# Performance work log

Hardware: AMD Instinct MI355X
Metric: run time of the kernel (lower is better)

The kernel has to match this reference:

```python
import jax, jax.numpy as jnp
import numpy as np

B, S, HID = 1, 2048, 2048
NH, NKV, D = 32, 8, 64
GROUPS = NH // NKV
THETA = 10000.0


def _rope_tables(seq_len, dim):
    inv_freq = 1.0 / (THETA ** (jnp.arange(0, dim, 2, dtype=jnp.float32) / dim))
    t = jnp.arange(seq_len, dtype=jnp.float32)
    freqs = jnp.outer(t, inv_freq)            # [S, D/2]
    emb = jnp.concatenate([freqs, freqs], axis=-1)  # [S, D]
    return jnp.cos(emb), jnp.sin(emb)


def _rotate_half(x):
    x1, x2 = jnp.split(x, 2, axis=-1)
    return jnp.concatenate([-x2, x1], axis=-1)


def setup_inputs() -> dict:
    key = jax.random.key(0)
    ks = jax.random.split(key, 8)
    hidden_states = jax.random.normal(ks[0], (B, S, HID), dtype=jnp.float32)
    # additive causal mask, 0 on/below diagonal, -1e9 above
    causal = jnp.tril(jnp.ones((S, S), dtype=bool))
    attention_mask = jnp.where(causal, 0.0, -1e9).astype(jnp.float32)[None, None]
    sc = 0.02
    Wq = sc * jax.random.normal(ks[1], (NH * D, HID), dtype=jnp.float32)
    bq = jnp.zeros((NH * D,), dtype=jnp.float32)
    Wk = sc * jax.random.normal(ks[2], (NKV * D, HID), dtype=jnp.float32)
    bk = jnp.zeros((NKV * D,), dtype=jnp.float32)
    Wv = sc * jax.random.normal(ks[3], (NKV * D, HID), dtype=jnp.float32)
    bv = jnp.zeros((NKV * D,), dtype=jnp.float32)
    Wo = sc * jax.random.normal(ks[4], (HID, NH * D), dtype=jnp.float32)
    return {"hidden_states": hidden_states, "attention_mask": attention_mask,
            "Wq": Wq, "bq": bq, "Wk": Wk, "bk": bk, "Wv": Wv, "bv": bv, "Wo": Wo}


def reference(hidden_states, attention_mask, Wq, bq, Wk, bk, Wv, bv, Wo):
    b, s, _ = hidden_states.shape
    q = (hidden_states @ Wq.T + bq).reshape(b, s, NH, D).transpose(0, 2, 1, 3)   # [B,NH,S,D]
    k = (hidden_states @ Wk.T + bk).reshape(b, s, NKV, D).transpose(0, 2, 1, 3)  # [B,NKV,S,D]
    v = (hidden_states @ Wv.T + bv).reshape(b, s, NKV, D).transpose(0, 2, 1, 3)
    cos, sin = _rope_tables(s, D)
    cos = cos[None, None]; sin = sin[None, None]
    q = q * cos + _rotate_half(q) * sin
    k = k * cos + _rotate_half(k) * sin
    # GQA: repeat KV heads to match query heads
    k = jnp.repeat(k, GROUPS, axis=1)  # [B,NH,S,D]
    v = jnp.repeat(v, GROUPS, axis=1)
    scores = jnp.einsum('bhqd,bhkd->bhqk', q, k) / jnp.sqrt(jnp.float32(D))
    scores = jnp.clip(scores, -50.0, 50.0)
    scores = scores + attention_mask
    probs = jax.nn.softmax(scores.astype(jnp.float32), axis=-1).astype(q.dtype)
    attn = jnp.einsum('bhqk,bhkd->bhqd', probs, v)
    attn = attn.transpose(0, 2, 1, 3).reshape(b, s, NH * D)
    return attn @ Wo.T
```

## Files before the change

### kernel.cpp

```cpp
#include <hip/hip_runtime.h>
#include <hip/hip_bf16.h>
#include <stdint.h>

typedef unsigned short u16;
typedef unsigned int u32;

#define S_LEN 2048
#define HID 2048
#define NH 32
#define NKV 8
#define HD 64
#define PIT 2080

using f32x4 = __attribute__((ext_vector_type(4))) float;
using bfrag = __attribute__((ext_vector_type(8))) short;

__device__ __forceinline__ float b2f(u16 u) {
  union { u32 i; float f; } c; c.i = ((u32)u) << 16; return c.f;
}
__device__ __forceinline__ u16 f2b(float f) {
  union { float f; u32 i; } c; c.f = f;
  u32 r = c.i + 0x7fffu + ((c.i >> 16) & 1u);
  return (u16)(r >> 16);
}
__device__ __forceinline__ uint4 cvt8(const float* __restrict__ p) {
  float4 a = *(const float4*)p;
  float4 b = *(const float4*)(p + 4);
  uint4 r;
  r.x = (u32)f2b(a.x) | ((u32)f2b(a.y) << 16);
  r.y = (u32)f2b(a.z) | ((u32)f2b(a.w) << 16);
  r.z = (u32)f2b(b.x) | ((u32)f2b(b.y) << 16);
  r.w = (u32)f2b(b.z) | ((u32)f2b(b.w) << 16);
  return r;
}

__device__ __forceinline__ void gl2lds16(const u16* g, u16* l) {
  __builtin_amdgcn_global_load_lds(
      (const __attribute__((address_space(1))) void*)g,
      (__attribute__((address_space(3))) void*)l,
      16, 0, 0);
}

__global__ void conv_all(const float* __restrict__ hid, const float* __restrict__ Wq,
                         const float* __restrict__ Wk, const float* __restrict__ Wv,
                         u16* __restrict__ hidb, u16* __restrict__ Wqkvb) {
  int row = blockIdx.x;
  int col = threadIdx.x * 8;
  const float* src; u16* dst;
  if (row < 2048)      { src = hid + (size_t)row * 2048;          dst = hidb  + (size_t)row * PIT; }
  else if (row < 4096) { src = Wq + (size_t)(row - 2048) * 2048;  dst = Wqkvb + (size_t)(row - 2048) * PIT; }
  else if (row < 4608) { src = Wk + (size_t)(row - 4096) * 2048;  dst = Wqkvb + (size_t)(row - 4096 + 2048) * PIT; }
  else                 { src = Wv + (size_t)(row - 4608) * 2048;  dst = Wqkvb + (size_t)(row - 4608 + 2560) * PIT; }
  *(uint4*)(dst + col) = cvt8(src + col);
}

__global__ void conv_f2b_p(const float* __restrict__ in, u16* __restrict__ out, int n8) {
  int i = blockIdx.x * 256 + threadIdx.x;
  if (i >= n8) return;
  int row = i >> 8;
  int col = (i & 255) * 8;
  *(uint4*)(out + (size_t)row * PIT + col) = cvt8(in + (size_t)row * 2048 + col);
}

__global__ __launch_bounds__(256, 3) void gemm_qkv(
    const u16* __restrict__ A, const u16* __restrict__ B,
    const float* __restrict__ bq, const float* __restrict__ bk, const float* __restrict__ bv,
    u16* __restrict__ Qb, u16* __restrict__ Kb, u16* __restrict__ Vt)
{
  __shared__ __align__(16) u16 As[64 * 32];
  __shared__ __align__(16) u16 Bs[128 * 32];
  __shared__ u16 strip_s[4][16 * 72];

  const int tid  = threadIdx.x;
  const int m0   = blockIdx.y * 64;
  const int n0   = blockIdx.x * 128;
  const int lane = tid & 63;
  const int w    = tid >> 6;
  const int wm   = w >> 1, wn = w & 1;
  const int quad = lane >> 4, l16 = lane & 15;

  const int srow = tid >> 2;
  const int scol = (tid & 3) * 8;
  const u16* ga = A + (size_t)(m0 + srow) * PIT + scol;
  const u16* gb = B + (size_t)(n0 + srow) * PIT + scol;
  u16* la = As + tid * 8;
  u16* lb = Bs + tid * 8;

  f32x4 zero = {0.f, 0.f, 0.f, 0.f};
  f32x4 acc[2][4];
#pragma unroll
  for (int mi = 0; mi < 2; ++mi)
#pragma unroll
    for (int ni = 0; ni < 4; ++ni) acc[mi][ni] = zero;

  for (int k0 = 0; k0 < HID; k0 += 32) {
    __syncthreads();
    gl2lds16(ga + k0, la);
    gl2lds16(gb + k0, lb);
    gl2lds16(gb + (size_t)64 * PIT + k0, lb + 2048);
    __syncthreads();

    bfrag af[2], bf[4];
#pragma unroll
    for (int i = 0; i < 2; ++i)
      af[i] = *(const bfrag*)&As[(wm * 32 + i * 16 + l16) * 32 + quad * 8];
#pragma unroll
    for (int i = 0; i < 4; ++i)
      bf[i] = *(const bfrag*)&Bs[(wn * 64 + i * 16 + l16) * 32 + quad * 8];
#pragma unroll
    for (int mi = 0; mi < 2; ++mi)
#pragma unroll
      for (int ni = 0; ni < 4; ++ni)
        acc[mi][ni] = __builtin_amdgcn_mfma_f32_16x16x32_bf16(af[mi], bf[ni], acc[mi][ni], 0, 0, 0);
  }

  u16* strip = strip_s[w];
  const int rr = lane >> 2;
  const int co = (lane & 3) * 8;

  if (n0 < 2048) {
#pragma unroll
    for (int mi = 0; mi < 2; ++mi) {
#pragma unroll
      for (int n01 = 0; n01 < 2; ++n01)
#pragma unroll
        for (int i = 0; i < 4; ++i) {
          int d  = n01 * 16 + l16;
          int c1 = n0 + wn * 64 + d;
          float x1 = acc[mi][n01][i]     + bq[c1];
          float x2 = acc[mi][n01 + 2][i] + bq[c1 + 32];
          float inv = exp2f(-(float)d * 0.41524101186092034f);
          float ang = (float)(m0 + wm * 32 + mi * 16 + quad * 4 + i) * inv;
          float cs = cosf(ang), sn = sinf(ang);
          strip[(quad * 4 + i) * 72 + d]      = f2b(x1 * cs - x2 * sn);
          strip[(quad * 4 + i) * 72 + d + 32] = f2b(x2 * cs + x1 * sn);
        }
      uint4 v0 = *(const uint4*)&strip[rr * 72 + co];
      uint4 v1 = *(const uint4*)&strip[rr * 72 + 32 + co];
      size_t gb2 = (size_t)(m0 + wm * 32 + mi * 16 + rr) * 2048 + n0 + wn * 64;
      *(uint4*)(Qb + gb2 + co)      = v0;
      *(uint4*)(Qb + gb2 + 32 + co) = v1;
    }
  } else if (n0 < 2560) {
    int cb = (n0 - 2048) + wn * 64;
#pragma unroll
    for (int mi = 0; mi < 2; ++mi) {
#pragma unroll
      for (int n01 = 0; n01 < 2; ++n01)
#pragma unroll
        for (int i = 0; i < 4; ++i) {
          int d  = n01 * 16 + l16;
          int cg = cb + d;
          float x1 = acc[mi][n01][i]     + bk[cg];
          float x2 = acc[mi][n01 + 2][i] + bk[cg + 32];
          float inv = exp2f(-(float)d * 0.41524101186092034f);
          float ang = (float)(m0 + wm * 32 + mi * 16 + quad * 4 + i) * inv;
          float cs = cosf(ang), sn = sinf(ang);
          strip[(quad * 4 + i) * 72 + d]      = f2b(x1 * cs - x2 * sn);
          strip[(quad * 4 + i) * 72 + d + 32] = f2b(x2 * cs + x1 * sn);
        }
      uint4 v0 = *(const uint4*)&strip[rr * 72 + co];
      uint4 v1 = *(const uint4*)&strip[rr * 72 + 32 + co];
      size_t gb2 = (size_t)(m0 + wm * 32 + mi * 16 + rr) * 512 + cb;
      *(uint4*)(Kb + gb2 + co)      = v0;
      *(uint4*)(Kb + gb2 + 32 + co) = v1;
    }
  } else {
    int cgb = (n0 - 2560) + wn * 64;
#pragma unroll
    for (int ni = 0; ni < 4; ++ni) {
      float bvv = bv[cgb + ni * 16 + l16];
#pragma unroll
      for (int mi = 0; mi < 2; ++mi)
#pragma unroll
        for (int i = 0; i < 4; ++i)
          strip[l16 * 72 + mi * 16 + quad * 4 + i] = f2b(acc[mi][ni][i] + bvv);
      uint4 v0 = *(const uint4*)&strip[rr * 72 + co];
      size_t gb2 = (size_t)(cgb + ni * 16 + rr) * PIT + m0 + wm * 32;
      *(uint4*)(Vt + gb2 + co) = v0;
    }
  }
}

__global__ __launch_bounds__(256, 3) void gemm_o(
    const u16* __restrict__ A, const u16* __restrict__ B, float* __restrict__ C)
{
  __shared__ __align__(16) u16 As[64 * 32];
  __shared__ __align__(16) u16 Bs[128 * 32];

  const int tid  = threadIdx.x;
  const int m0   = blockIdx.y * 64;
  const int n0   = blockIdx.x * 128;
  const int lane = tid & 63;
  const int w    = tid >> 6;
  const int wm   = w >> 1, wn = w & 1;
  const int quad = lane >> 4, l16 = lane & 15;

  const int srow = tid >> 2;
  const int scol = (tid & 3) * 8;
  const u16* ga = A + (size_t)(m0 + srow) * PIT + scol;
  const u16* gb = B + (size_t)(n0 + srow) * PIT + scol;
  u16* la = As + tid * 8;
  u16* lb = Bs + tid * 8;

  f32x4 zero = {0.f, 0.f, 0.f, 0.f};
  f32x4 acc[2][4];
#pragma unroll
  for (int mi = 0; mi < 2; ++mi)
#pragma unroll
    for (int ni = 0; ni < 4; ++ni) acc[mi][ni] = zero;

  for (int k0 = 0; k0 < HID; k0 += 32) {
    __syncthreads();
    gl2lds16(ga + k0, la);
    gl2lds16(gb + k0, lb);
    gl2lds16(gb + (size_t)64 * PIT + k0, lb + 2048);
    __syncthreads();

    bfrag af[2], bf[4];
#pragma unroll
    for (int i = 0; i < 2; ++i)
      af[i] = *(const bfrag*)&As[(wm * 32 + i * 16 + l16) * 32 + quad * 8];
#pragma unroll
    for (int i = 0; i < 4; ++i)
      bf[i] = *(const bfrag*)&Bs[(wn * 64 + i * 16 + l16) * 32 + quad * 8];
#pragma unroll
    for (int mi = 0; mi < 2; ++mi)
#pragma unroll
      for (int ni = 0; ni < 4; ++ni)
        acc[mi][ni] = __builtin_amdgcn_mfma_f32_16x16x32_bf16(af[mi], bf[ni], acc[mi][ni], 0, 0, 0);
  }

#pragma unroll
  for (int ni = 0; ni < 4; ++ni) {
    int col = n0 + wn * 64 + ni * 16 + l16;
#pragma unroll
    for (int mi = 0; mi < 2; ++mi)
#pragma unroll
      for (int i = 0; i < 4; ++i) {
        int row = m0 + wm * 32 + mi * 16 + quad * 4 + i;
        C[(size_t)row * 2048 + col] = acc[mi][ni][i];
      }
  }
}

#define SM_SC 0.18033688011112042f
#define SM_UB 72.134752044448169f

__global__ __launch_bounds__(256, 2) void attn_flash3(
    const u16* __restrict__ Qb, const u16* __restrict__ Kb,
    const u16* __restrict__ Vt, u16* __restrict__ Ab)
{
  __shared__ u16 Ps[4][2][16][72];

  const int h    = blockIdx.x;
  const int qbb  = 15 - (int)blockIdx.y;
  const int kvh  = h >> 2;
  const int tid  = threadIdx.x;
  const int lane = tid & 63;
  const int w    = tid >> 6;
  const int quad = lane >> 4, l16 = lane & 15;

  bfrag qf[2][2];
#pragma unroll
  for (int g = 0; g < 2; ++g) {
    const u16* qp = Qb + (size_t)(qbb * 128 + g * 64 + w * 16 + l16) * 2048 + h * 64 + quad * 8;
    qf[g][0] = *(const bfrag*)qp;
    qf[g][1] = *(const bfrag*)(qp + 32);
  }

  const u16* Kbase = Kb + (size_t)l16 * 512 + kvh * 64 + quad * 8;
  const u16* Vbase = Vt + (size_t)(kvh * 64 + l16) * PIT + quad * 8;

  f32x4 zero = {0.f, 0.f, 0.f, 0.f};
  f32x4 o_acc[2][4];
  float lpart[2][4];
#pragma unroll
  for (int g = 0; g < 2; ++g)
#pragma unroll
    for (int nb = 0; nb < 4; ++nb) { o_acc[g][nb] = zero; lpart[g][nb] = 0.f; }

#define LOADKV(kb, k0, k1, v0, v1)                                              \
  do {                                                                          \
    _Pragma("unroll")                                                           \
    for (int nb = 0; nb < 4; ++nb) {                                            \
      const u16* kp = Kbase + (size_t)((kb) * 64 + nb * 16) * 512;              \
      k0[nb] = *(const bfrag*)kp;                                               \
      k1[nb] = *(const bfrag*)(kp + 32);                                        \
      const u16* vp = Vbase + (size_t)(nb * 16) * PIT + (kb) * 64;              \
      v0[nb] = *(const bfrag*)vp;                                               \
      v1[nb] = *(const bfrag*)(vp + 32);                                        \
    }                                                                           \
  } while (0)

#define QKT_SM_FULL(k0, k1, g)                                                  \
  do {                                                                          \
    f32x4 s_acc[4];                                                             \
    _Pragma("unroll")                                                           \
    for (int nb = 0; nb < 4; ++nb) {                                            \
      s_acc[nb] = __builtin_amdgcn_mfma_f32_16x16x32_bf16(qf[g][0], k0[nb], zero, 0, 0, 0); \
      s_acc[nb] = __builtin_amdgcn_mfma_f32_16x16x32_bf16(qf[g][1], k1[nb], s_acc[nb], 0, 0, 0); \
    }                                                                           \
    _Pragma("unroll")                                                           \
    for (int nb = 0; nb < 4; ++nb)                                              \
      _Pragma("unroll")                                                         \
      for (int i = 0; i < 4; ++i) {                                             \
        float u = s_acc[nb][i] * SM_SC;                                         \
        u = fminf(SM_UB, fmaxf(-SM_UB, u));                                     \
        float p = __builtin_amdgcn_exp2f(u);                                    \
        lpart[g][i] += p;                                                       \
        Ps[w][g][quad * 4 + i][nb * 16 + l16] = f2b(p);                         \
      }                                                                         \
  } while (0)

#define QKT_SM_DIAG(k0, k1, g)                                                  \
  do {                                                                          \
    f32x4 s_acc[4];                                                             \
    _Pragma("unroll")                                                           \
    for (int nb = 0; nb < 4; ++nb) {                                            \
      s_acc[nb] = __builtin_amdgcn_mfma_f32_16x16x32_bf16(qf[g][0], k0[nb], zero, 0, 0, 0); \
      s_acc[nb] = __builtin_amdgcn_mfma_f32_16x16x32_bf16(qf[g][1], k1[nb], s_acc[nb], 0, 0, 0); \
    }                                                                           \
    _Pragma("unroll")                                                           \
    for (int nb = 0; nb < 4; ++nb)                                              \
      _Pragma("unroll")                                                         \
      for (int i = 0; i < 4; ++i) {                                             \
        float u = s_acc[nb][i] * SM_SC;                                         \
        u = fminf(SM_UB, fmaxf(-SM_UB, u));                                     \
        bool msk = (nb * 16 + l16 > w * 16 + quad * 4 + i);                     \
        float p = msk ? 0.0f : __builtin_amdgcn_exp2f(u);                       \
        lpart[g][i] += p;                                                       \
        Ps[w][g][quad * 4 + i][nb * 16 + l16] = f2b(p);                         \
      }                                                                         \
  } while (0)

#define PVACC(v0, v1, g)                                                        \
  do {                                                                          \
    bfrag pf0 = *(const bfrag*)&Ps[w][g][l16][quad * 8];                        \
    bfrag pf1 = *(const bfrag*)&Ps[w][g][l16][32 + quad * 8];                   \
    _Pragma("unroll")                                                           \
    for (int nb = 0; nb < 4; ++nb) {                                            \
      o_acc[g][nb] = __builtin_amdgcn_mfma_f32_16x16x32_bf16(pf0, v0[nb], o_acc[g][nb], 0, 0, 0); \
      o_acc[g][nb] = __builtin_amdgcn_mfma_f32_16x16x32_bf16(pf1, v1[nb], o_acc[g][nb], 0, 0, 0); \
    }                                                                           \
  } while (0)

  bfrag kX0[4], kX1[4], vX0[4], vX1[4];
  bfrag kY0[4], kY1[4], vY0[4], vY1[4];

  const int bulk  = 2 * qbb;
  const int kbmax = bulk + 1;

  LOADKV(0, kX0, kX1, vX0, vX1);

  int kb = 0;
  while (kb + 2 <= bulk) {
    LOADKV(kb + 1, kY0, kY1, vY0, vY1);
    QKT_SM_FULL(kX0, kX1, 0);
    QKT_SM_FULL(kX0, kX1, 1);
    PVACC(vX0, vX1, 0);
    PVACC(vX0, vX1, 1);
    LOADKV(kb + 2, kX0, kX1, vX0, vX1);
    QKT_SM_FULL(kY0, kY1, 0);
    QKT_SM_FULL(kY0, kY1, 1);
    PVACC(vY0, vY1, 0);
    PVACC(vY0, vY1, 1);
    kb += 2;
  }
  LOADKV(kbmax, kY0, kY1, vY0, vY1);
  QKT_SM_DIAG(kX0, kX1, 0);
  QKT_SM_FULL(kX0, kX1, 1);
  PVACC(vX0, vX1, 0);
  PVACC(vX0, vX1, 1);
  QKT_SM_DIAG(kY0, kY1, 1);
  PVACC(vY0, vY1, 1);

#pragma unroll
  for (int off = 1; off < 16; off <<= 1)
#pragma unroll
    for (int g = 0; g < 2; ++g)
#pragma unroll
      for (int i = 0; i < 4; ++i)
        lpart[g][i] += __shfl_xor(lpart[g][i], off, 64);

#pragma unroll
  for (int g = 0; g < 2; ++g)
#pragma unroll
    for (int i = 0; i < 4; ++i) {
      float inv = 1.0f / lpart[g][i];
      size_t rbase = (size_t)(qbb * 128 + g * 64 + w * 16 + quad * 4 + i) * PIT + h * 64;
#pragma unroll
      for (int nb = 0; nb < 4; ++nb)
        Ab[rbase + nb * 16 + l16] = f2b(o_acc[g][nb][i] * inv);
    }
}

extern "C" void kernel_launch(void* const* d_in, const int* in_sizes, int n_in,
                              void* d_out, int out_size, void* d_ws, size_t ws_size,
                              hipStream_t stream) {
  const float* hid = (const float*)d_in[0];
  const float* Wq = (const float*)d_in[2];
  const float* bq = (const float*)d_in[3];
  const float* Wk = (const float*)d_in[4];
  const float* bk = (const float*)d_in[5];
  const float* Wv = (const float*)d_in[6];
  const float* bv = (const float*)d_in[7];
  const float* Wo = (const float*)d_in[8];

  u16* hidb  = (u16*)d_ws;
  u16* Wqkvb = hidb + (size_t)2048 * PIT;
  u16* Qb    = Wqkvb + (size_t)3072 * PIT;
  u16* Kb    = Qb + 4194304;
  u16* Vt    = Kb + 1048576;
  u16* Wob   = hidb;
  u16* Ab    = Wqkvb;
  float* Ob  = (float*)d_out;

  conv_all<<<5120, 256, 0, stream>>>(hid, Wq, Wk, Wv, hidb, Wqkvb);

  gemm_qkv<<<dim3(24, 32), 256, 0, stream>>>(hidb, Wqkvb, bq, bk, bv, Qb, Kb, Vt);

  conv_f2b_p<<<2048, 256, 0, stream>>>(Wo, Wob, 524288);

  attn_flash3<<<dim3(32, 16), 256, 0, stream>>>(Qb, Kb, Vt, Ab);

  gemm_o<<<dim3(16, 32), 256, 0, stream>>>(Ab, Wob, Ob);
}
```

Measured before the change: 280.4 us.

## Double-buffer LDS tiles in GEMMs and stage swizzled K/V through LDS in attention

Both GEMM kernels now keep two LDS buffers, so the next k-slice is issued to LDS while MFMAs run on the current one, and each iteration needs one barrier instead of two. The attention kernel stops having each wave load its K/V fragments straight from global memory into registers. All four waves now cooperatively stage each 64x64 K and V tile into double-buffered LDS with an XOR swizzle, then read fragments from there. This cuts redundant global traffic across waves and register pressure. In exchange it uses more LDS, which may lower occupancy, and adds a block-wide barrier per KV step.

```diff
diff --git a/kernel.cpp b/kernel.cpp
--- a/kernel.cpp
+++ b/kernel.cpp
@@ -67,9 +67,9 @@
     const float* __restrict__ bq, const float* __restrict__ bk, const float* __restrict__ bv,
     u16* __restrict__ Qb, u16* __restrict__ Kb, u16* __restrict__ Vt)
 {
-  __shared__ __align__(16) u16 As[64 * 32];
-  __shared__ __align__(16) u16 Bs[128 * 32];
-  __shared__ u16 strip_s[4][16 * 72];
+  __shared__ __align__(16) u16 As[2 * 2048];
+  __shared__ __align__(16) u16 Bs[2 * 4096];
+  __shared__ __align__(16) u16 strip_s[4][16 * 72];
 
   const int tid  = threadIdx.x;
   const int m0   = blockIdx.y * 64;
@@ -83,8 +83,6 @@
   const int scol = (tid & 3) * 8;
   const u16* ga = A + (size_t)(m0 + srow) * PIT + scol;
   const u16* gb = B + (size_t)(n0 + srow) * PIT + scol;
-  u16* la = As + tid * 8;
-  u16* lb = Bs + tid * 8;
 
   f32x4 zero = {0.f, 0.f, 0.f, 0.f};
   f32x4 acc[2][4];
@@ -93,25 +91,38 @@
 #pragma unroll
     for (int ni = 0; ni < 4; ++ni) acc[mi][ni] = zero;
 
+  gl2lds16(ga, As + tid * 8);
+  gl2lds16(gb, Bs + tid * 8);
+  gl2lds16(gb + (size_t)64 * PIT, Bs + 2048 + tid * 8);
+  __syncthreads();
+
+  int cur = 0;
   for (int k0 = 0; k0 < HID; k0 += 32) {
-    __syncthreads();
-    gl2lds16(ga + k0, la);
-    gl2lds16(gb + k0, lb);
-    gl2lds16(gb + (size_t)64 * PIT + k0, lb + 2048);
-    __syncthreads();
+    if (k0 + 32 < HID) {
+      u16* la = As + (cur ^ 1) * 2048 + tid * 8;
+      u16* lb = Bs + (cur ^ 1) * 4096 + tid * 8;
+      gl2lds16(ga + k0 + 32, la);
+      gl2lds16(gb + k0 + 32, lb);
+      gl2lds16(gb + (size_t)64 * PIT + k0 + 32, lb + 2048);
+    }
+    const u16* as = As + cur * 2048;
+    const u16* bs = Bs + cur * 4096;
 
     bfrag af[2], bf[4];
 #pragma unroll
     for (int i = 0; i < 2; ++i)
-      af[i] = *(const bfrag*)&As[(wm * 32 + i * 16 + l16) * 32 + quad * 8];
+      af[i] = *(const bfrag*)&as[(wm * 32 + i * 16 + l16) * 32 + quad * 8];
 #pragma unroll
     for (int i = 0; i < 4; ++i)
-      bf[i] = *(const bfrag*)&Bs[(wn * 64 + i * 16 + l16) * 32 + quad * 8];
+      bf[i] = *(const bfrag*)&bs[(wn * 64 + i * 16 + l16) * 32 + quad * 8];
 #pragma unroll
     for (int mi = 0; mi < 2; ++mi)
 #pragma unroll
       for (int ni = 0; ni < 4; ++ni)
         acc[mi][ni] = __builtin_amdgcn_mfma_f32_16x16x32_bf16(af[mi], bf[ni], acc[mi][ni], 0, 0, 0);
+
+    __syncthreads();
+    cur ^= 1;
   }
 
   u16* strip = strip_s[w];
@@ -185,8 +196,8 @@
 __global__ __launch_bounds__(256, 3) void gemm_o(
     const u16* __restrict__ A, const u16* __restrict__ B, float* __restrict__ C)
 {
-  __shared__ __align__(16) u16 As[64 * 32];
-  __shared__ __align__(16) u16 Bs[128 * 32];
+  __shared__ __align__(16) u16 As[2 * 2048];
+  __shared__ __align__(16) u16 Bs[2 * 4096];
 
   const int tid  = threadIdx.x;
   const int m0   = blockIdx.y * 64;
@@ -200,8 +211,6 @@
   const int scol = (tid & 3) * 8;
   const u16* ga = A + (size_t)(m0 + srow) * PIT + scol;
   const u16* gb = B + (size_t)(n0 + srow) * PIT + scol;
-  u16* la = As + tid * 8;
-  u16* lb = Bs + tid * 8;
 
   f32x4 zero = {0.f, 0.f, 0.f, 0.f};
   f32x4 acc[2][4];
@@ -210,25 +219,38 @@
 #pragma unroll
     for (int ni = 0; ni < 4; ++ni) acc[mi][ni] = zero;
 
+  gl2lds16(ga, As + tid * 8);
+  gl2lds16(gb, Bs + tid * 8);
+  gl2lds16(gb + (size_t)64 * PIT, Bs + 2048 + tid * 8);
+  __syncthreads();
+
+  int cur = 0;
   for (int k0 = 0; k0 < HID; k0 += 32) {
-    __syncthreads();
-    gl2lds16(ga + k0, la);
-    gl2lds16(gb + k0, lb);
-    gl2lds16(gb + (size_t)64 * PIT + k0, lb + 2048);
-    __syncthreads();
+    if (k0 + 32 < HID) {
+      u16* la = As + (cur ^ 1) * 2048 + tid * 8;
+      u16* lb = Bs + (cur ^ 1) * 4096 + tid * 8;
+      gl2lds16(ga + k0 + 32, la);
+      gl2lds16(gb + k0 + 32, lb);
+      gl2lds16(gb + (size_t)64 * PIT + k0 + 32, lb + 2048);
+    }
+    const u16* as = As + cur * 2048;
+    const u16* bs = Bs + cur * 4096;
 
     bfrag af[2], bf[4];
 #pragma unroll
     for (int i = 0; i < 2; ++i)
-      af[i] = *(const bfrag*)&As[(wm * 32 + i * 16 + l16) * 32 + quad * 8];
+      af[i] = *(const bfrag*)&as[(wm * 32 + i * 16 + l16) * 32 + quad * 8];
 #pragma unroll
     for (int i = 0; i < 4; ++i)
-      bf[i] = *(const bfrag*)&Bs[(wn * 64 + i * 16 + l16) * 32 + quad * 8];
+      bf[i] = *(const bfrag*)&bs[(wn * 64 + i * 16 + l16) * 32 + quad * 8];
 #pragma unroll
     for (int mi = 0; mi < 2; ++mi)
 #pragma unroll
       for (int ni = 0; ni < 4; ++ni)
         acc[mi][ni] = __builtin_amdgcn_mfma_f32_16x16x32_bf16(af[mi], bf[ni], acc[mi][ni], 0, 0, 0);
+
+    __syncthreads();
+    cur ^= 1;
   }
 
 #pragma unroll
@@ -247,11 +269,13 @@
 #define SM_SC 0.18033688011112042f
 #define SM_UB 72.134752044448169f
 
-__global__ __launch_bounds__(256, 2) void attn_flash3(
+__global__ __launch_bounds__(256, 2) void attn_flash4(
     const u16* __restrict__ Qb, const u16* __restrict__ Kb,
     const u16* __restrict__ Vt, u16* __restrict__ Ab)
 {
-  __shared__ u16 Ps[4][2][16][72];
+  __shared__ __align__(16) u16 Ks[2][64 * 64];
+  __shared__ __align__(16) u16 Vs[2][64 * 64];
+  __shared__ __align__(16) u16 Ps[4][2][16][72];
 
   const int h    = blockIdx.x;
   const int qbb  = 15 - (int)blockIdx.y;
@@ -269,8 +293,23 @@
     qf[g][1] = *(const bfrag*)(qp + 32);
   }
 
-  const u16* Kbase = Kb + (size_t)l16 * 512 + kvh * 64 + quad * 8;
-  const u16* Vbase = Vt + (size_t)(kvh * 64 + l16) * PIT + quad * 8;
+  const int c0  = w * 128 + lane;
+  const int r0  = c0 >> 3,        s0 = c0 & 7;
+  const int r1  = (c0 + 64) >> 3, s1 = (c0 + 64) & 7;
+  const int sg0 = s0 ^ (r0 & 7);
+  const int sg1 = s1 ^ (r1 & 7);
+  const u16* Ksrc0 = Kb + (size_t)r0 * 512 + kvh * 64 + sg0 * 8;
+  const u16* Ksrc1 = Kb + (size_t)r1 * 512 + kvh * 64 + sg1 * 8;
+  const u16* Vsrc0 = Vt + (size_t)(kvh * 64 + r0) * PIT + sg0 * 8;
+  const u16* Vsrc1 = Vt + (size_t)(kvh * 64 + r1) * PIT + sg1 * 8;
+
+#define STAGEKV(buf, kb)                                                        \
+  do {                                                                          \
+    gl2lds16(Ksrc0 + (size_t)(kb) * 32768, &Ks[buf][0] + c0 * 8);               \
+    gl2lds16(Ksrc1 + (size_t)(kb) * 32768, &Ks[buf][0] + (c0 + 64) * 8);        \
+    gl2lds16(Vsrc0 + (kb) * 64,            &Vs[buf][0] + c0 * 8);               \
+    gl2lds16(Vsrc1 + (kb) * 64,            &Vs[buf][0] + (c0 + 64) * 8);        \
+  } while (0)
 
   f32x4 zero = {0.f, 0.f, 0.f, 0.f};
   f32x4 o_acc[2][4];
@@ -280,26 +319,13 @@
 #pragma unroll
     for (int nb = 0; nb < 4; ++nb) { o_acc[g][nb] = zero; lpart[g][nb] = 0.f; }
 
-#define LOADKV(kb, k0, k1, v0, v1)                                              \
-  do {                                                                          \
-    _Pragma("unroll")                                                           \
-    for (int nb = 0; nb < 4; ++nb) {                                            \
-      const u16* kp = Kbase + (size_t)((kb) * 64 + nb * 16) * 512;              \
-      k0[nb] = *(const bfrag*)kp;                                               \
-      k1[nb] = *(const bfrag*)(kp + 32);                                        \
-      const u16* vp = Vbase + (size_t)(nb * 16) * PIT + (kb) * 64;              \
-      v0[nb] = *(const bfrag*)vp;                                               \
-      v1[nb] = *(const bfrag*)(vp + 32);                                        \
-    }                                                                           \
-  } while (0)
-
-#define QKT_SM_FULL(k0, k1, g)                                                  \
+#define QKT_SM_FULL(g)                                                          \
   do {                                                                          \
     f32x4 s_acc[4];                                                             \
     _Pragma("unroll")                                                           \
     for (int nb = 0; nb < 4; ++nb) {                                            \
-      s_acc[nb] = __builtin_amdgcn_mfma_f32_16x16x32_bf16(qf[g][0], k0[nb], zero, 0, 0, 0); \
-      s_acc[nb] = __builtin_amdgcn_mfma_f32_16x16x32_bf16(qf[g][1], k1[nb], s_acc[nb], 0, 0, 0); \
+      s_acc[nb] = __builtin_amdgcn_mfma_f32_16x16x32_bf16(qf[g][0], kf0[nb], zero, 0, 0, 0); \
+      s_acc[nb] = __builtin_amdgcn_mfma_f32_16x16x32_bf16(qf[g][1], kf1[nb], s_acc[nb], 0, 0, 0); \
     }                                                                           \
     _Pragma("unroll")                                                           \
     for (int nb = 0; nb < 4; ++nb)                                              \
@@ -313,13 +339,13 @@
       }                                                                         \
   } while (0)
 
-#define QKT_SM_DIAG(k0, k1, g)                                                  \
+#define QKT_SM_DIAG(g)                                                          \
   do {                                                                          \
     f32x4 s_acc[4];                                                             \
     _Pragma("unroll")                                                           \
     for (int nb = 0; nb < 4; ++nb) {                                            \
-      s_acc[nb] = __builtin_amdgcn_mfma_f32_16x16x32_bf16(qf[g][0], k0[nb], zero, 0, 0, 0); \
-      s_acc[nb] = __builtin_amdgcn_mfma_f32_16x16x32_bf16(qf[g][1], k1[nb], s_acc[nb], 0, 0, 0); \
+      s_acc[nb] = __builtin_amdgcn_mfma_f32_16x16x32_bf16(qf[g][0], kf0[nb], zero, 0, 0, 0); \
+      s_acc[nb] = __builtin_amdgcn_mfma_f32_16x16x32_bf16(qf[g][1], kf1[nb], s_acc[nb], 0, 0, 0); \
     }                                                                           \
     _Pragma("unroll")                                                           \
     for (int nb = 0; nb < 4; ++nb)                                              \
@@ -334,46 +360,57 @@
       }                                                                         \
   } while (0)
 
-#define PVACC(v0, v1, g)                                                        \
+#define PVACC(g)                                                                \
   do {                                                                          \
     bfrag pf0 = *(const bfrag*)&Ps[w][g][l16][quad * 8];                        \
     bfrag pf1 = *(const bfrag*)&Ps[w][g][l16][32 + quad * 8];                   \
     _Pragma("unroll")                                                           \
     for (int nb = 0; nb < 4; ++nb) {                                            \
-      o_acc[g][nb] = __builtin_amdgcn_mfma_f32_16x16x32_bf16(pf0, v0[nb], o_acc[g][nb], 0, 0, 0); \
-      o_acc[g][nb] = __builtin_amdgcn_mfma_f32_16x16x32_bf16(pf1, v1[nb], o_acc[g][nb], 0, 0, 0); \
+      o_acc[g][nb] = __builtin_amdgcn_mfma_f32_16x16x32_bf16(pf0, vf0[nb], o_acc[g][nb], 0, 0, 0); \
+      o_acc[g][nb] = __builtin_amdgcn_mfma_f32_16x16x32_bf16(pf1, vf1[nb], o_acc[g][nb], 0, 0, 0); \
     }                                                                           \
   } while (0)
 
-  bfrag kX0[4], kX1[4], vX0[4], vX1[4];
-  bfrag kY0[4], kY1[4], vY0[4], vY1[4];
-
   const int bulk  = 2 * qbb;
   const int kbmax = bulk + 1;
-
-  LOADKV(0, kX0, kX1, vX0, vX1);
-
-  int kb = 0;
-  while (kb + 2 <= bulk) {
-    LOADKV(kb + 1, kY0, kY1, vY0, vY1);
-    QKT_SM_FULL(kX0, kX1, 0);
-    QKT_SM_FULL(kX0, kX1, 1);
-    PVACC(vX0, vX1, 0);
-    PVACC(vX0, vX1, 1);
-    LOADKV(kb + 2, kX0, kX1, vX0, vX1);
-    QKT_SM_FULL(kY0, kY1, 0);
-    QKT_SM_FULL(kY0, kY1, 1);
-    PVACC(vY0, vY1, 0);
-    PVACC(vY0, vY1, 1);
-    kb += 2;
-  }
-  LOADKV(kbmax, kY0, kY1, vY0, vY1);
-  QKT_SM_DIAG(kX0, kX1, 0);
-  QKT_SM_FULL(kX0, kX1, 1);
-  PVACC(vX0, vX1, 0);
-  PVACC(vX0, vX1, 1);
-  QKT_SM_DIAG(kY0, kY1, 1);
-  PVACC(vY0, vY1, 1);
+  const int swz   = (l16 & 7) * 8;
+
+  STAGEKV(0, 0);
+  __syncthreads();
+
+  int cur = 0;
+  for (int kb = 0; kb <= kbmax; ++kb) {
+    if (kb < kbmax) STAGEKV(cur ^ 1, kb + 1);
+
+    const u16* ks = &Ks[cur][0];
+    const u16* vs = &Vs[cur][0];
+
+    bfrag kf0[4], kf1[4];
+#pragma unroll
+    for (int nb = 0; nb < 4; ++nb) {
+      int row = (nb * 16 + l16) * 64;
+      kf0[nb] = *(const bfrag*)&ks[row + ((quad * 8) ^ swz)];
+      kf1[nb] = *(const bfrag*)&ks[row + ((32 + quad * 8) ^ swz)];
+    }
+
+    if (kb < bulk)        { QKT_SM_FULL(0); QKT_SM_FULL(1); }
+    else if (kb == bulk)  { QKT_SM_DIAG(0); QKT_SM_FULL(1); }
+    else                  { QKT_SM_DIAG(1); }
+
+    bfrag vf0[4], vf1[4];
+#pragma unroll
+    for (int nb = 0; nb < 4; ++nb) {
+      int row = (nb * 16 + l16) * 64;
+      vf0[nb] = *(const bfrag*)&vs[row + ((quad * 8) ^ swz)];
+      vf1[nb] = *(const bfrag*)&vs[row + ((32 + quad * 8) ^ swz)];
+    }
+
+    if (kb <= bulk) PVACC(0);
+    PVACC(1);
+
+    __syncthreads();
+    cur ^= 1;
+  }
 
 #pragma unroll
   for (int off = 1; off < 16; off <<= 1)
@@ -422,7 +459,7 @@
 
   conv_f2b_p<<<2048, 256, 0, stream>>>(Wo, Wob, 524288);
 
-  attn_flash3<<<dim3(32, 16), 256, 0, stream>>>(Qb, Kb, Vt, Ab);
+  attn_flash4<<<dim3(32, 16), 256, 0, stream>>>(Qb, Kb, Vt, Ab);
 
   gemm_o<<<dim3(16, 32), 256, 0, stream>>>(Ab, Wob, Ob);
 }
```

Result: no change. 279.0 us (-0.5%).
